# Kernel optimization log

Measured on AMD Instinct MI355X. Metric: run time of the kernel, lower is better.

Reference implementation:

```python
import jax, jax.numpy as jnp
import numpy as np

B, NR, M, NL = 1, 384, 4, 128
IN_C, MID_C, OUT_C = 384, 32, 128


def setup_inputs() -> dict:
    key = jax.random.key(0)
    ks = jax.random.split(key, 24)
    s = 0.02
    d = {
        'rec_1d': jax.random.normal(ks[0], (B, NR, IN_C), jnp.float32),
        'lig_1d': jax.random.normal(ks[1], (B, M, NL, IN_C), jnp.float32),
        'pw_rep': jax.random.normal(ks[2], (B, NR + NL, NR + NL, OUT_C), jnp.float32),
        'rl1_w': jax.random.normal(ks[3], (MID_C, IN_C), jnp.float32) * s,
        'rl1_b': jax.random.normal(ks[4], (MID_C,), jnp.float32) * s,
        'rl2_w': jax.random.normal(ks[5], (MID_C, IN_C), jnp.float32) * s,
        'rl2_b': jax.random.normal(ks[6], (MID_C,), jnp.float32) * s,
        'll1_w': jax.random.normal(ks[7], (MID_C, IN_C), jnp.float32) * s,
        'll1_b': jax.random.normal(ks[8], (MID_C,), jnp.float32) * s,
        'll2_w': jax.random.normal(ks[9], (MID_C, IN_C), jnp.float32) * s,
        'll2_b': jax.random.normal(ks[10], (MID_C,), jnp.float32) * s,
        'rr_w': jax.random.normal(ks[11], (OUT_C, MID_C * MID_C), jnp.float32) * s,
        'rr_b': jax.random.normal(ks[12], (OUT_C,), jnp.float32) * s,
        'rl_w': jax.random.normal(ks[13], (OUT_C, MID_C * MID_C), jnp.float32) * s,
        'rl_b': jax.random.normal(ks[14], (OUT_C,), jnp.float32) * s,
        'lr_w': jax.random.normal(ks[15], (OUT_C, MID_C * MID_C), jnp.float32) * s,
        'lr_b': jax.random.normal(ks[16], (OUT_C,), jnp.float32) * s,
        'll_w': jax.random.normal(ks[17], (OUT_C, MID_C * MID_C), jnp.float32) * s,
        'll_b': jax.random.normal(ks[18], (OUT_C,), jnp.float32) * s,
    }
    return d


def reference(rec_1d, lig_1d, pw_rep,
              rl1_w, rl1_b, rl2_w, rl2_b,
              ll1_w, ll1_b, ll2_w, ll2_b,
              rr_w, rr_b, rl_w, rl_b, lr_w, lr_b, ll_w, ll_b):
    mid_c = rl1_w.shape[0]
    m = lig_1d.shape[1]

    # 1D projections (nn.Linear: x @ W.T + b)
    r_i = rec_1d @ rl1_w.T + rl1_b          # [b, NR, mid]
    r_j = rec_1d @ rl2_w.T + rl2_b          # [b, NR, mid]
    l_i = lig_1d @ ll1_w.T + ll1_b          # [b, m, NL, mid]
    l_j = lig_1d @ ll2_w.T + ll2_b          # [b, m, NL, mid]

    # final Linear weights over flattened (x, y) -> [out, x, y] (y fastest, matching .view)
    Wrr = rr_w.reshape(-1, mid_c, mid_c)
    Wrl = rl_w.reshape(-1, mid_c, mid_c)
    Wlr = lr_w.reshape(-1, mid_c, mid_c)
    Wll = ll_w.reshape(-1, mid_c, mid_c)

    # rr[b,i,j,o] = sum_xy r_i[b,i,x] r_j[b,j,y] Wrr[o,x,y]
    # contract projection weight with one factor first (OpenFold trick):
    rr = jnp.einsum('bioy,bjy->bijo', jnp.einsum('bix,oxy->bioy', r_i, Wrr), r_j) + rr_b

    # mean over m commutes with the broadcast outer products for rl/lr
    l_j_mean = l_j.mean(axis=1)             # [b, NL, mid]
    l_i_mean = l_i.mean(axis=1)             # [b, NL, mid]

    rl = jnp.einsum('bioy,bjy->bijo', jnp.einsum('bix,oxy->bioy', r_i, Wrl), l_j_mean) + rl_b

    # lr output is [b, j_lig, i_res, o]: x-axis from r_j, y-axis from l_i
    lr = jnp.einsum('bioy,bjy->bjio', jnp.einsum('bix,oxy->bioy', r_j, Wlr), l_i_mean) + lr_b

    # ll: mean over m of per-copy outer products (not separable)
    ll = jnp.einsum('bmioy,bmjy->bijo', jnp.einsum('bmix,oxy->bmioy', l_i, Wll), l_j) / m + ll_b

    top = jnp.concatenate([rr, rl], axis=2)  # [b, NR, NR+NL, out]
    bot = jnp.concatenate([lr, ll], axis=2)  # [b, NL, NR+NL, out]
    pw_update = jnp.concatenate([top, bot], axis=1).astype(pw_rep.dtype)
    return pw_update
```

## Files before the change

### kernel.cpp

```cpp
#include <hip/hip_runtime.h>

#define NRES 384
#define NLIG 128
#define INC 384
#define OUTC 128
#define NTOT 512

#define WS_RI   0
#define WS_RJ   12288
#define WS_LI   24576
#define WS_LJ   40960
#define WS_BF16 57344

#define BT_RR   0
#define BT_RL   1572864
#define BT_LR   3145728
#define BT_LL   4718592
#define BF_RJ   6815744
#define BF_LJM  6828032
#define BF_LIM  6832128
#define BF_LJ   6836224
#define BF_RI   6852608
#define BF_LI   6864896
#define BW_W    6881280

typedef __bf16 bf16x8 __attribute__((ext_vector_type(8)));
typedef __bf16 bf16x4 __attribute__((ext_vector_type(4)));
typedef float  f32x4  __attribute__((ext_vector_type(4)));

__device__ inline bf16x8 cvt8(const float* p) {
  f32x4 a = *(const f32x4*)p, b = *(const f32x4*)(p + 4);
  bf16x8 r;
  r[0] = (__bf16)a[0]; r[1] = (__bf16)a[1]; r[2] = (__bf16)a[2]; r[3] = (__bf16)a[3];
  r[4] = (__bf16)b[0]; r[5] = (__bf16)b[1]; r[6] = (__bf16)b[2]; r[7] = (__bf16)b[3];
  return r;
}

#define KW_STR 257
__global__ __launch_bounds__(256) void kP_proj(
    const float* __restrict__ rec, const float* __restrict__ lig,
    const float* __restrict__ rl1w, const float* __restrict__ rl1b,
    const float* __restrict__ rl2w, const float* __restrict__ rl2b,
    const float* __restrict__ ll1w, const float* __restrict__ ll1b,
    const float* __restrict__ ll2w, const float* __restrict__ ll2b,
    const float* __restrict__ Wrr, const float* __restrict__ Wrl,
    const float* __restrict__ Wlr, const float* __restrict__ Wll,
    float* __restrict__ ws) {
  __shared__ float lds[32 * KW_STR];
  int b = blockIdx.x, t = threadIdx.x;
  __bf16* B16 = (__bf16*)(ws + WS_BF16);
  if (b >= 28) {
    int bb = b - 28;
    int tt = bb >> 4, oc = bb & 15;
    const float* W = tt == 0 ? Wrr : tt == 1 ? Wrl : tt == 2 ? Wlr : Wll;
    __bf16* Wb = B16 + BW_W + tt * 131072;
    int o0 = oc * 8;
#pragma unroll
    for (int it = 0; it < 32; ++it) {
      int idx = it * 256 + t;
      int oo = idx >> 10, r = idx & 1023;
      int x = r >> 5, y = r & 31;
      lds[x * KW_STR + oo * 32 + y] = W[(size_t)(o0 + oo) * 1024 + r];
    }
    __syncthreads();
#pragma unroll
    for (int it = 0; it < 32; ++it) {
      int idx = it * 256 + t;
      int x = idx & 31, nl = idx >> 5;
      Wb[(size_t)(o0 * 32 + nl) * 32 + x] = (__bf16)lds[x * KW_STR + nl];
    }
    return;
  }
  int l = t & 63, w = t >> 6;
  int lr16 = l & 15, lq = l >> 4;
  int pair = w >> 1, rh = w & 1;

  const float* in;
  const float *w1, *b1, *w2, *b2;
  float *o1, *o2;
  __bf16 *bf1, *bf2;
  int row0;
  if (b < 12) {
    row0 = b * 32;
    in = rec; w1 = rl1w; b1 = rl1b; w2 = rl2w; b2 = rl2b;
    o1 = ws + WS_RI; o2 = ws + WS_RJ;
    bf1 = B16 + BF_RI; bf2 = B16 + BF_RJ;
  } else {
    row0 = (b - 12) * 32;
    in = lig; w1 = ll1w; b1 = ll1b; w2 = ll2w; b2 = ll2b;
    o1 = ws + WS_LI; o2 = ws + WS_LJ;
    bf1 = B16 + BF_LI; bf2 = B16 + BF_LJ;
  }
  const float* wsrc = pair ? w2 : w1;
  const float* bsrc = pair ? b2 : b1;
  float* osrc = pair ? o2 : o1;
  __bf16* bdst = pair ? bf2 : bf1;
  int arow = row0 + rh * 16 + lr16;

  f32x4 acc[2];
#pragma unroll
  for (int ci = 0; ci < 2; ++ci) acc[ci] = (f32x4){0.f, 0.f, 0.f, 0.f};
  for (int ks = 0; ks < 12; ++ks) {
    bf16x8 af = cvt8(in + (size_t)arow * INC + ks * 32 + lq * 8);
#pragma unroll
    for (int ci = 0; ci < 2; ++ci) {
      int ch = ci * 16 + lr16;
      bf16x8 bf = cvt8(wsrc + (size_t)ch * INC + ks * 32 + lq * 8);
      acc[ci] = __builtin_amdgcn_mfma_f32_16x16x32_bf16(af, bf, acc[ci], 0, 0, 0);
    }
  }
#pragma unroll
  for (int ci = 0; ci < 2; ++ci) {
    int c = ci * 16 + lr16;
    float bias = bsrc[c];
#pragma unroll
    for (int e = 0; e < 4; ++e) {
      int r = row0 + rh * 16 + 4 * lq + e;
      float v = acc[ci][e] + bias;
      osrc[r * 32 + c] = v;
      bdst[r * 32 + c] = (__bf16)v;
    }
  }
}

__global__ __launch_bounds__(256) void k2_makeA(float* __restrict__ ws) {
  int b = blockIdx.x, t = threadIdx.x;
  __bf16* B16 = (__bf16*)(ws + WS_BF16);
  if (b >= 128) {
    const float* lj = ws + WS_LJ;
    const float* li = ws + WS_LI;
    __bf16* dm = B16 + BF_LJM;
    __bf16* di = B16 + BF_LIM;
    for (int k = 0; k < 16; ++k) {
      int idx = k * 256 + t;
      dm[idx] = (__bf16)(0.25f * (lj[idx] + lj[4096 + idx] + lj[8192 + idx] + lj[12288 + idx]));
      di[idx] = (__bf16)(0.25f * (li[idx] + li[4096 + idx] + li[8192 + idx] + li[12288 + idx]));
    }
    return;
  }
  int tt = b >> 5, sub = b & 31;
  int nt = sub >> 1, mh = sub & 1;
  const __bf16* facB;
  __bf16* At;
  int M;
  if (tt == 0)      { facB = B16 + BF_RI; At = B16 + BT_RR; M = 384; }
  else if (tt == 1) { facB = B16 + BF_RI; At = B16 + BT_RL; M = 384; }
  else if (tt == 2) { facB = B16 + BF_RJ; At = B16 + BT_LR; M = 384; }
  else              { facB = B16 + BF_LI; At = B16 + BT_LL; M = 512; }
  const __bf16* Wb = B16 + BW_W + tt * 131072;
  int l = t & 63, w = t >> 6;
  int lr16 = l & 15, lq = l >> 4;
  int n0w = nt * 256 + w * 64;
  int mtiles = (M >> 5);
  int m0 = mh * (M >> 1);

  bf16x8 wv[4];
#pragma unroll
  for (int q = 0; q < 4; ++q)
    wv[q] = *(const bf16x8*)(Wb + (size_t)(n0w + q * 16 + lr16) * 32 + lq * 8);

  for (int mt = 0; mt < mtiles; ++mt) {
    bf16x8 fv = *(const bf16x8*)(facB + (size_t)(m0 + mt * 16 + lr16) * 32 + lq * 8);
    f32x4 acc[4];
#pragma unroll
    for (int q = 0; q < 4; ++q) acc[q] = (f32x4){0.f, 0.f, 0.f, 0.f};
#pragma unroll
    for (int q = 0; q < 4; ++q)
      acc[q] = __builtin_amdgcn_mfma_f32_16x16x32_bf16(wv[q], fv, acc[q], 0, 0, 0);
    int m = m0 + mt * 16 + lr16;
#pragma unroll
    for (int q = 0; q < 4; ++q) {
      bf16x4 v;
#pragma unroll
      for (int e = 0; e < 4; ++e) v[e] = (__bf16)acc[q][e];
      *(bf16x4*)(At + (size_t)m * 4096 + n0w + q * 16 + 4 * lq) = v;
    }
  }
}

__global__ __launch_bounds__(256) void k3_mfma(
    const float* __restrict__ ws, float* __restrict__ out,
    const float* __restrict__ rrb, const float* __restrict__ rlb,
    const float* __restrict__ lrb, const float* __restrict__ llb) {
  const __bf16* B16 = (const __bf16*)(ws + WS_BF16);
  int b = blockIdx.x, t = threadIdx.x;
  int l = t & 63, w = t >> 6;
  int lr16 = l & 15, lq = l >> 4;

  if (b < 1920) {
    const __bf16* At;
    const __bf16* fc;
    const float* bias;
    float* outp;
    size_t jstr;
    if (b < 1152) {
      int i = b / 3, jt = b - 3 * i;
      At = B16 + BT_RR + (size_t)i * 4096;
      fc = B16 + BF_RJ + jt * 4096;
      bias = rrb; outp = out + ((size_t)i * NTOT + jt * 128) * OUTC; jstr = OUTC;
    } else if (b < 1536) {
      int i = b - 1152;
      At = B16 + BT_RL + (size_t)i * 4096;
      fc = B16 + BF_LJM;
      bias = rlb; outp = out + ((size_t)i * NTOT + NRES) * OUTC; jstr = OUTC;
    } else {
      int i = b - 1536;
      At = B16 + BT_LR + (size_t)i * 4096;
      fc = B16 + BF_LIM;
      bias = lrb; outp = out + (size_t)NRES * NTOT * OUTC + (size_t)i * OUTC;
      jstr = (size_t)NTOT * OUTC;
    }
    bf16x8 fj[2];
#pragma unroll
    for (int jj = 0; jj < 2; ++jj)
      fj[jj] = *(const bf16x8*)(fc + (size_t)(w * 32 + jj * 16 + lr16) * 32 + lq * 8);
    f32x4 acc[2][8];
#pragma unroll
    for (int jj = 0; jj < 2; ++jj)
#pragma unroll
      for (int ot = 0; ot < 8; ++ot) acc[jj][ot] = (f32x4){0.f, 0.f, 0.f, 0.f};
#pragma unroll
    for (int oc = 0; oc < 2; ++oc) {
      bf16x8 av[4];
#pragma unroll
      for (int o4 = 0; o4 < 4; ++o4)
        av[o4] = *(const bf16x8*)(At + (size_t)((oc * 4 + o4) * 16 + lr16) * 32 + lq * 8);
#pragma unroll
      for (int jj = 0; jj < 2; ++jj)
#pragma unroll
        for (int o4 = 0; o4 < 4; ++o4)
          acc[jj][oc * 4 + o4] =
              __builtin_amdgcn_mfma_f32_16x16x32_bf16(av[o4], fj[jj], acc[jj][oc * 4 + o4], 0, 0, 0);
    }
#pragma unroll
    for (int jj = 0; jj < 2; ++jj) {
      int j = w * 32 + jj * 16 + lr16;
#pragma unroll
      for (int ot = 0; ot < 8; ++ot) {
        f32x4 b4 = *(const f32x4*)&bias[ot * 16 + 4 * lq];
        f32x4 v = acc[jj][ot] + b4;
        *(f32x4*)&outp[(size_t)j * jstr + ot * 16 + 4 * lq] = v;
      }
    }
  } else {
    int il = b - 1920;
    f32x4 acc[2][8];
#pragma unroll
    for (int jj = 0; jj < 2; ++jj)
#pragma unroll
      for (int ot = 0; ot < 8; ++ot) acc[jj][ot] = (f32x4){0.f, 0.f, 0.f, 0.f};
    for (int m = 0; m < 4; ++m) {
      const __bf16* At = B16 + BT_LL + (size_t)(m * 128 + il) * 4096;
      const __bf16* fc = B16 + BF_LJ + m * 4096;
      bf16x8 fj[2];
#pragma unroll
      for (int jj = 0; jj < 2; ++jj)
        fj[jj] = *(const bf16x8*)(fc + (size_t)(w * 32 + jj * 16 + lr16) * 32 + lq * 8);
#pragma unroll
      for (int oc = 0; oc < 2; ++oc) {
        bf16x8 av[4];
#pragma unroll
        for (int o4 = 0; o4 < 4; ++o4)
          av[o4] = *(const bf16x8*)(At + (size_t)((oc * 4 + o4) * 16 + lr16) * 32 + lq * 8);
#pragma unroll
        for (int jj = 0; jj < 2; ++jj)
#pragma unroll
          for (int o4 = 0; o4 < 4; ++o4)
            acc[jj][oc * 4 + o4] =
                __builtin_amdgcn_mfma_f32_16x16x32_bf16(av[o4], fj[jj], acc[jj][oc * 4 + o4], 0, 0, 0);
      }
    }
    float* outp = out + ((size_t)(NRES + il) * NTOT + NRES) * OUTC;
#pragma unroll
    for (int jj = 0; jj < 2; ++jj) {
      int j = w * 32 + jj * 16 + lr16;
#pragma unroll
      for (int ot = 0; ot < 8; ++ot) {
        f32x4 b4 = *(const f32x4*)&llb[ot * 16 + 4 * lq];
        f32x4 v = 0.25f * acc[jj][ot] + b4;
        *(f32x4*)&outp[(size_t)j * OUTC + ot * 16 + 4 * lq] = v;
      }
    }
  }
}

extern "C" void kernel_launch(void* const* d_in, const int* in_sizes, int n_in,
                              void* d_out, int out_size, void* d_ws, size_t ws_size,
                              hipStream_t stream) {
  const float* rec  = (const float*)d_in[0];
  const float* lig  = (const float*)d_in[1];
  const float* rl1w = (const float*)d_in[3];
  const float* rl1b = (const float*)d_in[4];
  const float* rl2w = (const float*)d_in[5];
  const float* rl2b = (const float*)d_in[6];
  const float* ll1w = (const float*)d_in[7];
  const float* ll1b = (const float*)d_in[8];
  const float* ll2w = (const float*)d_in[9];
  const float* ll2b = (const float*)d_in[10];
  const float* rrw  = (const float*)d_in[11];
  const float* rrb  = (const float*)d_in[12];
  const float* rlw  = (const float*)d_in[13];
  const float* rlb  = (const float*)d_in[14];
  const float* lrw  = (const float*)d_in[15];
  const float* lrb  = (const float*)d_in[16];
  const float* llw  = (const float*)d_in[17];
  const float* llb  = (const float*)d_in[18];
  float* out = (float*)d_out;
  float* ws  = (float*)d_ws;

  hipLaunchKernelGGL(kP_proj, dim3(92), dim3(256), 0, stream,
                     rec, lig, rl1w, rl1b, rl2w, rl2b, ll1w, ll1b, ll2w, ll2b,
                     rrw, rlw, lrw, llw, ws);
  hipLaunchKernelGGL(k2_makeA, dim3(129), dim3(256), 0, stream, ws);
  hipLaunchKernelGGL(k3_mfma, dim3(2048), dim3(256), 0, stream,
                     ws, out, rrb, rlb, lrb, llb);
}
```

Baseline: 55.32 us.

## Fuse three kernels into one persistent kernel with grid-wide barriers

```diff
diff --git a/kernel.cpp b/kernel.cpp
--- a/kernel.cpp
+++ b/kernel.cpp
@@ -5,12 +5,14 @@
 #define INC 384
 #define OUTC 128
 #define NTOT 512
+#define GRID 256
 
 #define WS_RI   0
 #define WS_RJ   12288
 #define WS_LI   24576
 #define WS_LJ   40960
 #define WS_BF16 57344
+#define WS_CNT  3760128
 
 #define BT_RR   0
 #define BT_RL   1572864
@@ -24,6 +26,8 @@
 #define BF_LI   6864896
 #define BW_W    6881280
 
+#define KW_STR 257
+
 typedef __bf16 bf16x8 __attribute__((ext_vector_type(8)));
 typedef __bf16 bf16x4 __attribute__((ext_vector_type(4)));
 typedef float  f32x4  __attribute__((ext_vector_type(4)));
@@ -36,8 +40,21 @@
   return r;
 }
 
-#define KW_STR 257
-__global__ __launch_bounds__(256) void kP_proj(
+__device__ __forceinline__ void grid_barrier(unsigned* cnt, unsigned target) {
+  __syncthreads();
+  if (threadIdx.x == 0) {
+    __hip_atomic_fetch_add(cnt, 1u, __ATOMIC_ACQ_REL, __HIP_MEMORY_SCOPE_AGENT);
+    unsigned v;
+    do {
+      __builtin_amdgcn_s_sleep(2);
+      v = __hip_atomic_load(cnt, __ATOMIC_RELAXED, __HIP_MEMORY_SCOPE_AGENT);
+    } while (v < target);
+  }
+  __syncthreads();
+  __threadfence();
+}
+
+__global__ __launch_bounds__(256, 2) void fused_all(
     const float* __restrict__ rec, const float* __restrict__ lig,
     const float* __restrict__ rl1w, const float* __restrict__ rl1b,
     const float* __restrict__ rl2w, const float* __restrict__ rl2b,
@@ -45,11 +62,65 @@
     const float* __restrict__ ll2w, const float* __restrict__ ll2b,
     const float* __restrict__ Wrr, const float* __restrict__ Wrl,
     const float* __restrict__ Wlr, const float* __restrict__ Wll,
-    float* __restrict__ ws) {
+    const float* __restrict__ rrb, const float* __restrict__ rlb,
+    const float* __restrict__ lrb, const float* __restrict__ llb,
+    float* __restrict__ ws, float* __restrict__ out) {
   __shared__ float lds[32 * KW_STR];
+  unsigned* cnt = (unsigned*)(ws + WS_CNT);
   int b = blockIdx.x, t = threadIdx.x;
   __bf16* B16 = (__bf16*)(ws + WS_BF16);
-  if (b >= 28) {
+  int l = t & 63, w = t >> 6;
+  int lr16 = l & 15, lq = l >> 4;
+
+  if (b < 28) {
+    int pair = w >> 1, rh = w & 1;
+    const float* in;
+    const float *w1, *b1, *w2, *b2;
+    float *o1, *o2;
+    __bf16 *bf1, *bf2;
+    int row0;
+    if (b < 12) {
+      row0 = b * 32;
+      in = rec; w1 = rl1w; b1 = rl1b; w2 = rl2w; b2 = rl2b;
+      o1 = ws + WS_RI; o2 = ws + WS_RJ;
+      bf1 = B16 + BF_RI; bf2 = B16 + BF_RJ;
+    } else {
+      row0 = (b - 12) * 32;
+      in = lig; w1 = ll1w; b1 = ll1b; w2 = ll2w; b2 = ll2b;
+      o1 = ws + WS_LI; o2 = ws + WS_LJ;
+      bf1 = B16 + BF_LI; bf2 = B16 + BF_LJ;
+    }
+    const float* wsrc = pair ? w2 : w1;
+    const float* bsrc = pair ? b2 : b1;
+    float* osrc = pair ? o2 : o1;
+    __bf16* bdst = pair ? bf2 : bf1;
+    int arow = row0 + rh * 16 + lr16;
+
+    f32x4 acc[2];
+#pragma unroll
+    for (int ci = 0; ci < 2; ++ci) acc[ci] = (f32x4){0.f, 0.f, 0.f, 0.f};
+    for (int ks = 0; ks < 12; ++ks) {
+      bf16x8 af = cvt8(in + (size_t)arow * INC + ks * 32 + lq * 8);
+#pragma unroll
+      for (int ci = 0; ci < 2; ++ci) {
+        int ch = ci * 16 + lr16;
+        bf16x8 bf = cvt8(wsrc + (size_t)ch * INC + ks * 32 + lq * 8);
+        acc[ci] = __builtin_amdgcn_mfma_f32_16x16x32_bf16(af, bf, acc[ci], 0, 0, 0);
+      }
+    }
+#pragma unroll
+    for (int ci = 0; ci < 2; ++ci) {
+      int c = ci * 16 + lr16;
+      float bias = bsrc[c];
+#pragma unroll
+      for (int e = 0; e < 4; ++e) {
+        int r = row0 + rh * 16 + 4 * lq + e;
+        float v = acc[ci][e] + bias;
+        osrc[r * 32 + c] = v;
+        bdst[r * 32 + c] = (__bf16)v;
+      }
+    }
+  } else if (b < 92) {
     int bb = b - 28;
     int tt = bb >> 4, oc = bb & 15;
     const float* W = tt == 0 ? Wrr : tt == 1 ? Wrl : tt == 2 ? Wlr : Wll;
@@ -69,193 +140,94 @@
       int x = idx & 31, nl = idx >> 5;
       Wb[(size_t)(o0 * 32 + nl) * 32 + x] = (__bf16)lds[x * KW_STR + nl];
     }
-    return;
   }
-  int l = t & 63, w = t >> 6;
-  int lr16 = l & 15, lq = l >> 4;
-  int pair = w >> 1, rh = w & 1;
-
-  const float* in;
-  const float *w1, *b1, *w2, *b2;
-  float *o1, *o2;
-  __bf16 *bf1, *bf2;
-  int row0;
-  if (b < 12) {
-    row0 = b * 32;
-    in = rec; w1 = rl1w; b1 = rl1b; w2 = rl2w; b2 = rl2b;
-    o1 = ws + WS_RI; o2 = ws + WS_RJ;
-    bf1 = B16 + BF_RI; bf2 = B16 + BF_RJ;
-  } else {
-    row0 = (b - 12) * 32;
-    in = lig; w1 = ll1w; b1 = ll1b; w2 = ll2w; b2 = ll2b;
-    o1 = ws + WS_LI; o2 = ws + WS_LJ;
-    bf1 = B16 + BF_LI; bf2 = B16 + BF_LJ;
+  grid_barrier(cnt + 0, GRID);
+
+  for (int u = b; u < 257; u += GRID) {
+    if (u < 256) {
+      int tt = u >> 6, sub = u & 63;
+      int nt = sub >> 2, mq = sub & 3;
+      const __bf16* facB;
+      __bf16* At;
+      int M;
+      if (tt == 0)      { facB = B16 + BF_RI; At = B16 + BT_RR; M = 384; }
+      else if (tt == 1) { facB = B16 + BF_RI; At = B16 + BT_RL; M = 384; }
+      else if (tt == 2) { facB = B16 + BF_RJ; At = B16 + BT_LR; M = 384; }
+      else              { facB = B16 + BF_LI; At = B16 + BT_LL; M = 512; }
+      const __bf16* Wb = B16 + BW_W + tt * 131072;
+      int n0w = nt * 256 + w * 64;
+      int mtiles = M >> 6;
+      int m0 = mq * (M >> 2);
+
+      bf16x8 wv[4];
+#pragma unroll
+      for (int q = 0; q < 4; ++q)
+        wv[q] = *(const bf16x8*)(Wb + (size_t)(n0w + q * 16 + lr16) * 32 + lq * 8);
+
+      for (int mt = 0; mt < mtiles; ++mt) {
+        bf16x8 fv = *(const bf16x8*)(facB + (size_t)(m0 + mt * 16 + lr16) * 32 + lq * 8);
+        f32x4 acc[4];
+#pragma unroll
+        for (int q = 0; q < 4; ++q) acc[q] = (f32x4){0.f, 0.f, 0.f, 0.f};
+#pragma unroll
+        for (int q = 0; q < 4; ++q)
+          acc[q] = __builtin_amdgcn_mfma_f32_16x16x32_bf16(wv[q], fv, acc[q], 0, 0, 0);
+        int m = m0 + mt * 16 + lr16;
+#pragma unroll
+        for (int q = 0; q < 4; ++q) {
+          bf16x4 v;
+#pragma unroll
+          for (int e = 0; e < 4; ++e) v[e] = (__bf16)acc[q][e];
+          *(bf16x4*)(At + (size_t)m * 4096 + n0w + q * 16 + 4 * lq) = v;
+        }
+      }
+    } else {
+      const float* lj = ws + WS_LJ;
+      const float* li = ws + WS_LI;
+      __bf16* dm = B16 + BF_LJM;
+      __bf16* di = B16 + BF_LIM;
+      for (int k = 0; k < 16; ++k) {
+        int idx = k * 256 + t;
+        dm[idx] = (__bf16)(0.25f * (lj[idx] + lj[4096 + idx] + lj[8192 + idx] + lj[12288 + idx]));
+        di[idx] = (__bf16)(0.25f * (li[idx] + li[4096 + idx] + li[8192 + idx] + li[12288 + idx]));
+      }
+    }
   }
-  const float* wsrc = pair ? w2 : w1;
-  const float* bsrc = pair ? b2 : b1;
-  float* osrc = pair ? o2 : o1;
-  __bf16* bdst = pair ? bf2 : bf1;
-  int arow = row0 + rh * 16 + lr16;
-
-  f32x4 acc[2];
-#pragma unroll
-  for (int ci = 0; ci < 2; ++ci) acc[ci] = (f32x4){0.f, 0.f, 0.f, 0.f};
-  for (int ks = 0; ks < 12; ++ks) {
-    bf16x8 af = cvt8(in + (size_t)arow * INC + ks * 32 + lq * 8);
-#pragma unroll
-    for (int ci = 0; ci < 2; ++ci) {
-      int ch = ci * 16 + lr16;
-      bf16x8 bf = cvt8(wsrc + (size_t)ch * INC + ks * 32 + lq * 8);
-      acc[ci] = __builtin_amdgcn_mfma_f32_16x16x32_bf16(af, bf, acc[ci], 0, 0, 0);
-    }
-  }
-#pragma unroll
-  for (int ci = 0; ci < 2; ++ci) {
-    int c = ci * 16 + lr16;
-    float bias = bsrc[c];
-#pragma unroll
-    for (int e = 0; e < 4; ++e) {
-      int r = row0 + rh * 16 + 4 * lq + e;
-      float v = acc[ci][e] + bias;
-      osrc[r * 32 + c] = v;
-      bdst[r * 32 + c] = (__bf16)v;
-    }
-  }
-}
-
-__global__ __launch_bounds__(256) void k2_makeA(float* __restrict__ ws) {
-  int b = blockIdx.x, t = threadIdx.x;
-  __bf16* B16 = (__bf16*)(ws + WS_BF16);
-  if (b >= 128) {
-    const float* lj = ws + WS_LJ;
-    const float* li = ws + WS_LI;
-    __bf16* dm = B16 + BF_LJM;
-    __bf16* di = B16 + BF_LIM;
-    for (int k = 0; k < 16; ++k) {
-      int idx = k * 256 + t;
-      dm[idx] = (__bf16)(0.25f * (lj[idx] + lj[4096 + idx] + lj[8192 + idx] + lj[12288 + idx]));
-      di[idx] = (__bf16)(0.25f * (li[idx] + li[4096 + idx] + li[8192 + idx] + li[12288 + idx]));
-    }
-    return;
-  }
-  int tt = b >> 5, sub = b & 31;
-  int nt = sub >> 1, mh = sub & 1;
-  const __bf16* facB;
-  __bf16* At;
-  int M;
-  if (tt == 0)      { facB = B16 + BF_RI; At = B16 + BT_RR; M = 384; }
-  else if (tt == 1) { facB = B16 + BF_RI; At = B16 + BT_RL; M = 384; }
-  else if (tt == 2) { facB = B16 + BF_RJ; At = B16 + BT_LR; M = 384; }
-  else              { facB = B16 + BF_LI; At = B16 + BT_LL; M = 512; }
-  const __bf16* Wb = B16 + BW_W + tt * 131072;
-  int l = t & 63, w = t >> 6;
-  int lr16 = l & 15, lq = l >> 4;
-  int n0w = nt * 256 + w * 64;
-  int mtiles = (M >> 5);
-  int m0 = mh * (M >> 1);
-
-  bf16x8 wv[4];
-#pragma unroll
-  for (int q = 0; q < 4; ++q)
-    wv[q] = *(const bf16x8*)(Wb + (size_t)(n0w + q * 16 + lr16) * 32 + lq * 8);
-
-  for (int mt = 0; mt < mtiles; ++mt) {
-    bf16x8 fv = *(const bf16x8*)(facB + (size_t)(m0 + mt * 16 + lr16) * 32 + lq * 8);
-    f32x4 acc[4];
-#pragma unroll
-    for (int q = 0; q < 4; ++q) acc[q] = (f32x4){0.f, 0.f, 0.f, 0.f};
-#pragma unroll
-    for (int q = 0; q < 4; ++q)
-      acc[q] = __builtin_amdgcn_mfma_f32_16x16x32_bf16(wv[q], fv, acc[q], 0, 0, 0);
-    int m = m0 + mt * 16 + lr16;
-#pragma unroll
-    for (int q = 0; q < 4; ++q) {
-      bf16x4 v;
-#pragma unroll
-      for (int e = 0; e < 4; ++e) v[e] = (__bf16)acc[q][e];
-      *(bf16x4*)(At + (size_t)m * 4096 + n0w + q * 16 + 4 * lq) = v;
-    }
-  }
-}
-
-__global__ __launch_bounds__(256) void k3_mfma(
-    const float* __restrict__ ws, float* __restrict__ out,
-    const float* __restrict__ rrb, const float* __restrict__ rlb,
-    const float* __restrict__ lrb, const float* __restrict__ llb) {
-  const __bf16* B16 = (const __bf16*)(ws + WS_BF16);
-  int b = blockIdx.x, t = threadIdx.x;
-  int l = t & 63, w = t >> 6;
-  int lr16 = l & 15, lq = l >> 4;
-
-  if (b < 1920) {
-    const __bf16* At;
-    const __bf16* fc;
-    const float* bias;
-    float* outp;
-    size_t jstr;
-    if (b < 1152) {
-      int i = b / 3, jt = b - 3 * i;
-      At = B16 + BT_RR + (size_t)i * 4096;
-      fc = B16 + BF_RJ + jt * 4096;
-      bias = rrb; outp = out + ((size_t)i * NTOT + jt * 128) * OUTC; jstr = OUTC;
-    } else if (b < 1536) {
-      int i = b - 1152;
-      At = B16 + BT_RL + (size_t)i * 4096;
-      fc = B16 + BF_LJM;
-      bias = rlb; outp = out + ((size_t)i * NTOT + NRES) * OUTC; jstr = OUTC;
-    } else {
-      int i = b - 1536;
-      At = B16 + BT_LR + (size_t)i * 4096;
-      fc = B16 + BF_LIM;
-      bias = lrb; outp = out + (size_t)NRES * NTOT * OUTC + (size_t)i * OUTC;
-      jstr = (size_t)NTOT * OUTC;
-    }
-    bf16x8 fj[2];
-#pragma unroll
-    for (int jj = 0; jj < 2; ++jj)
-      fj[jj] = *(const bf16x8*)(fc + (size_t)(w * 32 + jj * 16 + lr16) * 32 + lq * 8);
-    f32x4 acc[2][8];
-#pragma unroll
-    for (int jj = 0; jj < 2; ++jj)
-#pragma unroll
-      for (int ot = 0; ot < 8; ++ot) acc[jj][ot] = (f32x4){0.f, 0.f, 0.f, 0.f};
-#pragma unroll
-    for (int oc = 0; oc < 2; ++oc) {
-      bf16x8 av[4];
-#pragma unroll
-      for (int o4 = 0; o4 < 4; ++o4)
-        av[o4] = *(const bf16x8*)(At + (size_t)((oc * 4 + o4) * 16 + lr16) * 32 + lq * 8);
-#pragma unroll
-      for (int jj = 0; jj < 2; ++jj)
-#pragma unroll
-        for (int o4 = 0; o4 < 4; ++o4)
-          acc[jj][oc * 4 + o4] =
-              __builtin_amdgcn_mfma_f32_16x16x32_bf16(av[o4], fj[jj], acc[jj][oc * 4 + o4], 0, 0, 0);
-    }
-#pragma unroll
-    for (int jj = 0; jj < 2; ++jj) {
-      int j = w * 32 + jj * 16 + lr16;
-#pragma unroll
-      for (int ot = 0; ot < 8; ++ot) {
-        f32x4 b4 = *(const f32x4*)&bias[ot * 16 + 4 * lq];
-        f32x4 v = acc[jj][ot] + b4;
-        *(f32x4*)&outp[(size_t)j * jstr + ot * 16 + 4 * lq] = v;
-      }
-    }
-  } else {
-    int il = b - 1920;
-    f32x4 acc[2][8];
-#pragma unroll
-    for (int jj = 0; jj < 2; ++jj)
-#pragma unroll
-      for (int ot = 0; ot < 8; ++ot) acc[jj][ot] = (f32x4){0.f, 0.f, 0.f, 0.f};
-    for (int m = 0; m < 4; ++m) {
-      const __bf16* At = B16 + BT_LL + (size_t)(m * 128 + il) * 4096;
-      const __bf16* fc = B16 + BF_LJ + m * 4096;
+  grid_barrier(cnt + 1, GRID);
+
+  for (int u = b; u < 2048; u += GRID) {
+    if (u < 1920) {
+      const __bf16* At;
+      const __bf16* fc;
+      const float* bias;
+      float* outp;
+      size_t jstr;
+      if (u < 1152) {
+        int i = u / 3, jt = u - 3 * i;
+        At = B16 + BT_RR + (size_t)i * 4096;
+        fc = B16 + BF_RJ + jt * 4096;
+        bias = rrb; outp = out + ((size_t)i * NTOT + jt * 128) * OUTC; jstr = OUTC;
+      } else if (u < 1536) {
+        int i = u - 1152;
+        At = B16 + BT_RL + (size_t)i * 4096;
+        fc = B16 + BF_LJM;
+        bias = rlb; outp = out + ((size_t)i * NTOT + NRES) * OUTC; jstr = OUTC;
+      } else {
+        int i = u - 1536;
+        At = B16 + BT_LR + (size_t)i * 4096;
+        fc = B16 + BF_LIM;
+        bias = lrb; outp = out + (size_t)NRES * NTOT * OUTC + (size_t)i * OUTC;
+        jstr = (size_t)NTOT * OUTC;
+      }
       bf16x8 fj[2];
 #pragma unroll
       for (int jj = 0; jj < 2; ++jj)
         fj[jj] = *(const bf16x8*)(fc + (size_t)(w * 32 + jj * 16 + lr16) * 32 + lq * 8);
+      f32x4 acc[2][8];
+#pragma unroll
+      for (int jj = 0; jj < 2; ++jj)
+#pragma unroll
+        for (int ot = 0; ot < 8; ++ot) acc[jj][ot] = (f32x4){0.f, 0.f, 0.f, 0.f};
 #pragma unroll
       for (int oc = 0; oc < 2; ++oc) {
         bf16x8 av[4];
@@ -269,16 +241,54 @@
             acc[jj][oc * 4 + o4] =
                 __builtin_amdgcn_mfma_f32_16x16x32_bf16(av[o4], fj[jj], acc[jj][oc * 4 + o4], 0, 0, 0);
       }
-    }
-    float* outp = out + ((size_t)(NRES + il) * NTOT + NRES) * OUTC;
-#pragma unroll
-    for (int jj = 0; jj < 2; ++jj) {
-      int j = w * 32 + jj * 16 + lr16;
-#pragma unroll
-      for (int ot = 0; ot < 8; ++ot) {
-        f32x4 b4 = *(const f32x4*)&llb[ot * 16 + 4 * lq];
-        f32x4 v = 0.25f * acc[jj][ot] + b4;
-        *(f32x4*)&outp[(size_t)j * OUTC + ot * 16 + 4 * lq] = v;
+#pragma unroll
+      for (int jj = 0; jj < 2; ++jj) {
+        int j = w * 32 + jj * 16 + lr16;
+#pragma unroll
+        for (int ot = 0; ot < 8; ++ot) {
+          f32x4 b4 = *(const f32x4*)&bias[ot * 16 + 4 * lq];
+          f32x4 v = acc[jj][ot] + b4;
+          *(f32x4*)&outp[(size_t)j * jstr + ot * 16 + 4 * lq] = v;
+        }
+      }
+    } else {
+      int il = u - 1920;
+      f32x4 acc[2][8];
+#pragma unroll
+      for (int jj = 0; jj < 2; ++jj)
+#pragma unroll
+        for (int ot = 0; ot < 8; ++ot) acc[jj][ot] = (f32x4){0.f, 0.f, 0.f, 0.f};
+      for (int m = 0; m < 4; ++m) {
+        const __bf16* At = B16 + BT_LL + (size_t)(m * 128 + il) * 4096;
+        const __bf16* fc = B16 + BF_LJ + m * 4096;
+        bf16x8 fj[2];
+#pragma unroll
+        for (int jj = 0; jj < 2; ++jj)
+          fj[jj] = *(const bf16x8*)(fc + (size_t)(w * 32 + jj * 16 + lr16) * 32 + lq * 8);
+#pragma unroll
+        for (int oc = 0; oc < 2; ++oc) {
+          bf16x8 av[4];
+#pragma unroll
+          for (int o4 = 0; o4 < 4; ++o4)
+            av[o4] = *(const bf16x8*)(At + (size_t)((oc * 4 + o4) * 16 + lr16) * 32 + lq * 8);
+#pragma unroll
+          for (int jj = 0; jj < 2; ++jj)
+#pragma unroll
+            for (int o4 = 0; o4 < 4; ++o4)
+              acc[jj][oc * 4 + o4] =
+                  __builtin_amdgcn_mfma_f32_16x16x32_bf16(av[o4], fj[jj], acc[jj][oc * 4 + o4], 0, 0, 0);
+        }
+      }
+      float* outp = out + ((size_t)(NRES + il) * NTOT + NRES) * OUTC;
+#pragma unroll
+      for (int jj = 0; jj < 2; ++jj) {
+        int j = w * 32 + jj * 16 + lr16;
+#pragma unroll
+        for (int ot = 0; ot < 8; ++ot) {
+          f32x4 b4 = *(const f32x4*)&llb[ot * 16 + 4 * lq];
+          f32x4 v = 0.25f * acc[jj][ot] + b4;
+          *(f32x4*)&outp[(size_t)j * OUTC + ot * 16 + 4 * lq] = v;
+        }
       }
     }
   }
@@ -308,10 +318,11 @@
   float* out = (float*)d_out;
   float* ws  = (float*)d_ws;
 
-  hipLaunchKernelGGL(kP_proj, dim3(92), dim3(256), 0, stream,
-                     rec, lig, rl1w, rl1b, rl2w, rl2b, ll1w, ll1b, ll2w, ll2b,
-                     rrw, rlw, lrw, llw, ws);
-  hipLaunchKernelGGL(k2_makeA, dim3(129), dim3(256), 0, stream, ws);
-  hipLaunchKernelGGL(k3_mfma, dim3(2048), dim3(256), 0, stream,
-                     ws, out, rrb, rlb, lrb, llb);
+  hipMemsetAsync((char*)d_ws + (size_t)WS_CNT * 4, 0, 64, stream);
+
+  hipLaunchKernelGGL(fused_all, dim3(GRID), dim3(256), 0, stream,
+                     rec, lig, rl1w, rl1b, rl2w, rl2b,
+                     ll1w, ll1b, ll2w, ll2b,
+                     rrw, rlw, lrw, llw,
+                     rrb, rlb, lrb, llb, ws, out);
 }
```

New measurement: 116.1 us. 2.1x slower.
